# Performance work log

Measured on AMD Instinct MI355X. Metric: run time of the kernel, lower is better.

## Reference

```python
import jax, jax.numpy as jnp
import numpy as np

EPS = 1e-5

def hardsigmoid(x):
    # torch F.hardsigmoid: clip(x/6 + 0.5, 0, 1)
    return jnp.clip(x / 6.0 + 0.5, 0.0, 1.0)

def setup_inputs() -> dict:
    T, B, D = 2048, 8, 1024
    key = jax.random.key(0)
    k1, k2 = jax.random.split(key)
    x = jax.random.normal(k1, (T, B, D), dtype=jnp.float32)
    c = jnp.zeros((B, D), dtype=jnp.float32)
    # params
    w_ufr = jax.random.normal(k2, (3 * D, D), dtype=jnp.float32) * (1.0 / np.sqrt(D))
    gamma = jnp.ones((D,), dtype=jnp.float32)
    beta = jnp.zeros((D,), dtype=jnp.float32)
    return {"x": x, "c": c, "w_ufr": w_ufr, "gamma": gamma, "beta": beta}

def reference(x, c, w_ufr, gamma, beta):
    residual = x
    # LayerNorm over last dim
    mu = jnp.mean(x, axis=-1, keepdims=True)
    var = jnp.mean(jnp.square(x - mu), axis=-1, keepdims=True)
    x_norm = (x - mu) * jax.lax.rsqrt(var + EPS) * gamma + beta
    # fused projection to u, f, r: (T,B,D) @ (D,3D)
    ufr = jnp.einsum('tbd,ed->tbe', x_norm, w_ufr)
    u, f, r = jnp.split(ufr, 3, axis=-1)
    f_gate = hardsigmoid(f)
    r_gate = hardsigmoid(r)
    # diagonal linear recurrence: c_t = f_t * c_{t-1} + (1 - f_t) * u_t
    def step(c_prev, inputs):
        ft, ut = inputs
        c_curr = ft * c_prev + (1.0 - ft) * ut
        return c_curr, c_curr
    c_last, c_all = jax.lax.scan(step, c, (f_gate, u))
    tanh_approx = c_all / (1.0 + jnp.abs(c_all))  # softsign
    hs = r_gate * tanh_approx + (1.0 - r_gate) * x_norm
    return (residual + hs, c_last)
```

## Files before the change

### kernel.cpp

```cpp
#include <hip/hip_runtime.h>
#include <stdint.h>


#define T_SEQ 2048
#define BATCH 8
#define DIM 1024
#define M_SZ (T_SEQ * BATCH)
#define N_SZ (3 * DIM)
#define K_SZ DIM
#define NCHUNK 32
#define CLEN (T_SEQ / NCHUNK)

#define GBM 256
#define GBN 256
#define GBK 32
#define NKT (K_SZ / GBK)
#define NBX (N_SZ / GBN)
#define NWG (NBX * (M_SZ / GBM))

typedef __attribute__((ext_vector_type(8))) __bf16 bf16x8;
typedef __attribute__((ext_vector_type(4))) float f32x4;

__device__ __forceinline__ unsigned short f2bf(float f) {
  unsigned int u = __float_as_uint(f);
  u += 0x7FFFu + ((u >> 16) & 1u);
  return (unsigned short)(u >> 16);
}
__device__ __forceinline__ float bf2f(unsigned short s) {
  return __uint_as_float(((unsigned int)s) << 16);
}
__device__ __forceinline__ void gload16(const void* g, void* l) {
  __builtin_amdgcn_global_load_lds(
      (__attribute__((address_space(1))) void*)const_cast<void*>(g),
      (__attribute__((address_space(3))) void*)l, 16, 0, 0);
}

__global__ __launch_bounds__(256) void cvt_kernel(const float* __restrict__ w,
                                                  unsigned short* __restrict__ wb) {
  const int i = blockIdx.x * 256 + threadIdx.x;
  const float4 v = reinterpret_cast<const float4*>(w)[i];
  ushort4 o;
  o.x = f2bf(v.x); o.y = f2bf(v.y); o.z = f2bf(v.z); o.w = f2bf(v.w);
  reinterpret_cast<ushort4*>(wb)[i] = o;
}

__global__ __launch_bounds__(256) void ln_kernel(const float* __restrict__ x,
                                                 const float* __restrict__ gamma,
                                                 const float* __restrict__ beta,
                                                 unsigned short* __restrict__ xn,
                                                 float* __restrict__ muO,
                                                 float* __restrict__ rsO) {
  const int row = blockIdx.x;
  const int tid = threadIdx.x;
  const float4 v = reinterpret_cast<const float4*>(x + (size_t)row * DIM)[tid];
  float s = v.x + v.y + v.z + v.w;
  float q = v.x * v.x + v.y * v.y + v.z * v.z + v.w * v.w;
#pragma unroll
  for (int off = 32; off > 0; off >>= 1) {
    s += __shfl_down(s, off);
    q += __shfl_down(q, off);
  }
  __shared__ float sbuf[8];
  const int wv = tid >> 6, ln = tid & 63;
  if (ln == 0) { sbuf[wv] = s; sbuf[4 + wv] = q; }
  __syncthreads();
  s = sbuf[0] + sbuf[1] + sbuf[2] + sbuf[3];
  q = sbuf[4] + sbuf[5] + sbuf[6] + sbuf[7];
  const float mu = s * (1.0f / DIM);
  const float rstd = rsqrtf(q * (1.0f / DIM) - mu * mu + 1e-5f);
  if (tid == 0) { muO[row] = mu; rsO[row] = rstd; }
  const float4 g = reinterpret_cast<const float4*>(gamma)[tid];
  const float4 b = reinterpret_cast<const float4*>(beta)[tid];
  ushort4 o;
  o.x = f2bf((v.x - mu) * rstd * g.x + b.x);
  o.y = f2bf((v.y - mu) * rstd * g.y + b.y);
  o.z = f2bf((v.z - mu) * rstd * g.z + b.z);
  o.w = f2bf((v.w - mu) * rstd * g.w + b.w);
  reinterpret_cast<ushort4*>(xn + (size_t)row * DIM)[tid] = o;
}

__global__ __launch_bounds__(512) void gemm_kernel(const unsigned short* __restrict__ A,
                                                   const unsigned short* __restrict__ W,
                                                   unsigned short* __restrict__ U,
                                                   unsigned char* __restrict__ Fq,
                                                   unsigned char* __restrict__ Rq) {
  __shared__ unsigned short smem[2 * 4 * GBM * GBK];
  const int tid = threadIdx.x;
  const int lane = tid & 63;
  const int wid = tid >> 6;
  const int wm = wid >> 2, wn = wid & 3;

  const int wg = (blockIdx.x & 7) * (NWG / 8) + (blockIdx.x >> 3);
  const int bn0 = (wg % NBX) * GBN;
  const int bm0 = (wg / NBX) * GBM;

  const int stgRow = wid * 32 + (lane >> 2);
  const int stgCol = ((lane & 3) ^ ((lane >> 3) & 3)) * 8;
  const unsigned short* gA = A + (size_t)(bm0 + stgRow) * K_SZ + stgCol;
  const unsigned short* gB = W + (size_t)(bn0 + stgRow) * K_SZ + stgCol;
  unsigned short* sAb = smem + wid * 32 * GBK;
  unsigned short* sBb = smem + 4 * GBM * GBK + wid * 32 * GBK;

#define STAGE(bufi, t) do {                                        \
    const size_t ko_ = (size_t)(t) * GBK;                          \
    unsigned short* sa_ = sAb + (bufi) * (GBM * GBK);              \
    unsigned short* sb_ = sBb + (bufi) * (GBM * GBK);              \
    gload16(gA + ko_, sa_);                                        \
    gload16(gA + ko_ + (size_t)16 * K_SZ, sa_ + 16 * GBK);         \
    gload16(gB + ko_, sb_);                                        \
    gload16(gB + ko_ + (size_t)16 * K_SZ, sb_ + 16 * GBK);         \
  } while (0)

  f32x4 acc[8][4] = {};
  const int fr = lane & 15;
  const int ko8 = ((lane >> 4) ^ ((fr >> 1) & 3)) * 8;

  STAGE(0, 0);
  STAGE(1, 1);
  STAGE(2, 2);
  asm volatile("s_waitcnt vmcnt(8)" ::: "memory");
  __builtin_amdgcn_s_barrier();
  asm volatile("" ::: "memory");

  for (int kt = 0; kt < NKT; ++kt) {
    const int cur = kt & 3;
    if (kt < NKT - 3) STAGE((kt + 3) & 3, kt + 3);

    const unsigned short* sa = smem + cur * (GBM * GBK);
    const unsigned short* sb = smem + 4 * GBM * GBK + cur * (GBM * GBK);
    bf16x8 af[8], bf[4];
#pragma unroll
    for (int i = 0; i < 8; i++)
      af[i] = *(const bf16x8*)&sa[(wm * 128 + i * 16 + fr) * GBK + ko8];
#pragma unroll
    for (int j = 0; j < 4; j++)
      bf[j] = *(const bf16x8*)&sb[(wn * 64 + j * 16 + fr) * GBK + ko8];

    __builtin_amdgcn_s_setprio(1);
#pragma unroll
    for (int i = 0; i < 8; i++)
#pragma unroll
      for (int j = 0; j < 4; j++)
        acc[i][j] = __builtin_amdgcn_mfma_f32_16x16x32_bf16(af[i], bf[j], acc[i][j], 0, 0, 0);
    __builtin_amdgcn_s_setprio(0);

    if (kt < NKT - 3)       asm volatile("s_waitcnt vmcnt(8)" ::: "memory");
    else if (kt == NKT - 3) asm volatile("s_waitcnt vmcnt(4)" ::: "memory");
    else if (kt == NKT - 2) asm volatile("s_waitcnt vmcnt(0)" ::: "memory");
    if (kt < NKT - 1) {
      __builtin_amdgcn_s_barrier();
      asm volatile("" ::: "memory");
    }
  }
#undef STAGE

  const int region = bn0 >> 10;
  const int cb0 = bn0 & 1023;
  const int fq = lane >> 4;
  unsigned char* G = (region == 1) ? Fq : Rq;
#pragma unroll
  for (int i = 0; i < 8; i++) {
#pragma unroll
    for (int j = 0; j < 4; j++) {
      const int coln = cb0 + wn * 64 + j * 16 + fr;
      size_t base = (size_t)(bm0 + wm * 128 + i * 16 + fq * 4) * DIM + coln;
      if (region == 0) {
#pragma unroll
        for (int r = 0; r < 4; r++)
          U[base + (size_t)r * DIM] = f2bf(acc[i][j][r]);
      } else {
#pragma unroll
        for (int r = 0; r < 4; r++) {
          float v = fminf(fmaxf(acc[i][j][r] * (1.0f / 6.0f) + 0.5f, 0.0f), 1.0f);
          G[base + (size_t)r * DIM] = (unsigned char)(v * 255.0f + 0.5f);
        }
      }
    }
  }
}

__global__ __launch_bounds__(256) void scan1_kernel(const unsigned short* __restrict__ U,
                                                    const unsigned char* __restrict__ Fq,
                                                    float* __restrict__ Ac,
                                                    float* __restrict__ Bc) {
  const int lin = blockIdx.x * 256 + threadIdx.x;
  const int d0 = (lin & 255) << 2;
  const int b = (lin >> 8) & (BATCH - 1);
  const int g = lin >> 11;
  size_t off = (size_t)(g * CLEN) * (BATCH * DIM) + (size_t)b * DIM + d0;
  float Aa0 = 1.0f, Aa1 = 1.0f, Aa2 = 1.0f, Aa3 = 1.0f;
  float Bb0 = 0.0f, Bb1 = 0.0f, Bb2 = 0.0f, Bb3 = 0.0f;
#pragma unroll 4
  for (int t = 0; t < CLEN; t++) {
    const ushort4 uu = *reinterpret_cast<const ushort4*>(&U[off]);
    const uchar4 ff = *reinterpret_cast<const uchar4*>(&Fq[off]);
    const float f0 = ff.x * (1.0f / 255.0f), f1 = ff.y * (1.0f / 255.0f);
    const float f2 = ff.z * (1.0f / 255.0f), f3 = ff.w * (1.0f / 255.0f);
    Aa0 *= f0; Aa1 *= f1; Aa2 *= f2; Aa3 *= f3;
    Bb0 = f0 * Bb0 + (1.0f - f0) * bf2f(uu.x);
    Bb1 = f1 * Bb1 + (1.0f - f1) * bf2f(uu.y);
    Bb2 = f2 * Bb2 + (1.0f - f2) * bf2f(uu.z);
    Bb3 = f3 * Bb3 + (1.0f - f3) * bf2f(uu.w);
    off += BATCH * DIM;
  }
  const int o = g * (BATCH * DIM) + b * DIM + d0;
  *reinterpret_cast<float4*>(&Ac[o]) = make_float4(Aa0, Aa1, Aa2, Aa3);
  *reinterpret_cast<float4*>(&Bc[o]) = make_float4(Bb0, Bb1, Bb2, Bb3);
}

__global__ __launch_bounds__(256) void scan2_kernel(const float* __restrict__ Ac,
                                                    const float* __restrict__ Bc,
                                                    const float* __restrict__ c0,
                                                    float* __restrict__ cstart,
                                                    float* __restrict__ clast) {
  const int lin = blockIdx.x * 256 + threadIdx.x;
  float c = c0[lin];
#pragma unroll
  for (int g = 0; g < NCHUNK; g++) {
    cstart[g * (BATCH * DIM) + lin] = c;
    c = Ac[g * (BATCH * DIM) + lin] * c + Bc[g * (BATCH * DIM) + lin];
  }
  clast[lin] = c;
}

__global__ __launch_bounds__(256) void scan3_kernel(const unsigned short* __restrict__ U,
                                                    const unsigned char* __restrict__ Fq,
                                                    const unsigned char* __restrict__ Rq,
                                                    const float* __restrict__ x,
                                                    const float* __restrict__ cstart,
                                                    const float* __restrict__ muA,
                                                    const float* __restrict__ rsA,
                                                    const float* __restrict__ gamma,
                                                    const float* __restrict__ beta,
                                                    float* __restrict__ out) {
  const int lin = blockIdx.x * 256 + threadIdx.x;
  const int d0 = (lin & 255) << 2;
  const int b = (lin >> 8) & (BATCH - 1);
  const int g = lin >> 11;
  const float4 cs = *reinterpret_cast<const float4*>(&cstart[g * (BATCH * DIM) + b * DIM + d0]);
  float c0 = cs.x, c1 = cs.y, c2 = cs.z, c3 = cs.w;
  const float4 gm = *reinterpret_cast<const float4*>(&gamma[d0]);
  const float4 bt = *reinterpret_cast<const float4*>(&beta[d0]);
  size_t xo = (size_t)(g * CLEN) * (BATCH * DIM) + (size_t)b * DIM + d0;
  int row = g * CLEN * BATCH + b;
#pragma unroll 2
  for (int t = 0; t < CLEN; t++) {
    const ushort4 uu = *reinterpret_cast<const ushort4*>(&U[xo]);
    const uchar4 ff = *reinterpret_cast<const uchar4*>(&Fq[xo]);
    const uchar4 rr = *reinterpret_cast<const uchar4*>(&Rq[xo]);
    const float4 xv = *reinterpret_cast<const float4*>(&x[xo]);
    const float mu = muA[row], rs = rsA[row];
    float o[4];
    {
      const float f = ff.x * (1.0f / 255.0f), r = rr.x * (1.0f / 255.0f);
      const float xnv = (xv.x - mu) * rs * gm.x + bt.x;
      c0 = f * c0 + (1.0f - f) * bf2f(uu.x);
      o[0] = xv.x + r * (c0 / (1.0f + fabsf(c0))) + (1.0f - r) * xnv;
    }
    {
      const float f = ff.y * (1.0f / 255.0f), r = rr.y * (1.0f / 255.0f);
      const float xnv = (xv.y - mu) * rs * gm.y + bt.y;
      c1 = f * c1 + (1.0f - f) * bf2f(uu.y);
      o[1] = xv.y + r * (c1 / (1.0f + fabsf(c1))) + (1.0f - r) * xnv;
    }
    {
      const float f = ff.z * (1.0f / 255.0f), r = rr.z * (1.0f / 255.0f);
      const float xnv = (xv.z - mu) * rs * gm.z + bt.z;
      c2 = f * c2 + (1.0f - f) * bf2f(uu.z);
      o[2] = xv.z + r * (c2 / (1.0f + fabsf(c2))) + (1.0f - r) * xnv;
    }
    {
      const float f = ff.w * (1.0f / 255.0f), r = rr.w * (1.0f / 255.0f);
      const float xnv = (xv.w - mu) * rs * gm.w + bt.w;
      c3 = f * c3 + (1.0f - f) * bf2f(uu.w);
      o[3] = xv.w + r * (c3 / (1.0f + fabsf(c3))) + (1.0f - r) * xnv;
    }
    *reinterpret_cast<float4*>(&out[xo]) = make_float4(o[0], o[1], o[2], o[3]);
    xo += BATCH * DIM;
    row += BATCH;
  }
}

extern "C" void kernel_launch(void* const* d_in, const int* in_sizes, int n_in,
                              void* d_out, int out_size, void* d_ws, size_t ws_size,
                              hipStream_t stream) {
  const float* x = (const float*)d_in[0];
  const float* c0 = (const float*)d_in[1];
  const float* w = (const float*)d_in[2];
  const float* gamma = (const float*)d_in[3];
  const float* beta = (const float*)d_in[4];
  float* out = (float*)d_out;
  float* clast = out + (size_t)M_SZ * DIM;

  char* ws = (char*)d_ws;
  unsigned short* xn = (unsigned short*)ws;
  unsigned short* U  = (unsigned short*)(ws + 33554432ull);
  unsigned char* Fq  = (unsigned char*)(ws + 67108864ull);
  unsigned char* Rq  = (unsigned char*)(ws + 83886080ull);
  float* Ac = (float*)(ws + 100663296ull);
  float* Bc = (float*)(ws + 101711872ull);
  float* cst = (float*)(ws + 102760448ull);
  unsigned short* wb = (unsigned short*)(ws + 103809024ull);
  float* muA = (float*)(ws + 110100480ull);
  float* rsA = (float*)(ws + 110166016ull);

  cvt_kernel<<<(N_SZ * K_SZ / 4) / 256, 256, 0, stream>>>(w, wb);
  ln_kernel<<<M_SZ, 256, 0, stream>>>(x, gamma, beta, xn, muA, rsA);
  gemm_kernel<<<NWG, 512, 0, stream>>>(xn, wb, U, Fq, Rq);
  scan1_kernel<<<(NCHUNK * BATCH * DIM / 4) / 256, 256, 0, stream>>>(U, Fq, Ac, Bc);
  scan2_kernel<<<(BATCH * DIM) / 256, 256, 0, stream>>>(Ac, Bc, c0, cst, clast);
  scan3_kernel<<<(NCHUNK * BATCH * DIM / 4) / 256, 256, 0, stream>>>(
      U, Fq, Rq, x, cst, muA, rsA, gamma, beta, out);
}
```

Baseline: 193.6 us.

## Fuse three-pass chunked scan into single-pass decoupled look-back kernel

Replaces the three scan kernels with one kernel in which each chunk block computes its local aggregate, publishes it with status flags, and looks back over predecessor chunks to get its starting state before producing outputs. The weight bf16 conversion and LayerNorm are also merged into one launch. This removes launch gaps and the intermediate cstart round trip, and it lets the U and F reads for the second pass hit cache. In exchange it relies on spin-waiting inter-block flags. The flags need all predecessor blocks to be resident or scheduled in order (256 blocks here), and there is an extra memset.

```diff
diff --git a/kernel.cpp b/kernel.cpp
--- a/kernel.cpp
+++ b/kernel.cpp
@@ -18,6 +18,8 @@
 #define NBX (N_SZ / GBN)
 #define NWG (NBX * (M_SZ / GBM))
 
+#define CVT_BLOCKS ((N_SZ * K_SZ / 4) / 256)
+
 typedef __attribute__((ext_vector_type(8))) __bf16 bf16x8;
 typedef __attribute__((ext_vector_type(4))) float f32x4;
 
@@ -35,23 +37,24 @@
       (__attribute__((address_space(3))) void*)l, 16, 0, 0);
 }
 
-__global__ __launch_bounds__(256) void cvt_kernel(const float* __restrict__ w,
-                                                  unsigned short* __restrict__ wb) {
-  const int i = blockIdx.x * 256 + threadIdx.x;
-  const float4 v = reinterpret_cast<const float4*>(w)[i];
-  ushort4 o;
-  o.x = f2bf(v.x); o.y = f2bf(v.y); o.z = f2bf(v.z); o.w = f2bf(v.w);
-  reinterpret_cast<ushort4*>(wb)[i] = o;
-}
-
-__global__ __launch_bounds__(256) void ln_kernel(const float* __restrict__ x,
-                                                 const float* __restrict__ gamma,
-                                                 const float* __restrict__ beta,
-                                                 unsigned short* __restrict__ xn,
-                                                 float* __restrict__ muO,
-                                                 float* __restrict__ rsO) {
-  const int row = blockIdx.x;
+__global__ __launch_bounds__(256) void prep_kernel(const float* __restrict__ w,
+                                                   unsigned short* __restrict__ wb,
+                                                   const float* __restrict__ x,
+                                                   const float* __restrict__ gamma,
+                                                   const float* __restrict__ beta,
+                                                   unsigned short* __restrict__ xn,
+                                                   float* __restrict__ muO,
+                                                   float* __restrict__ rsO) {
   const int tid = threadIdx.x;
+  if (blockIdx.x < CVT_BLOCKS) {
+    const int i = blockIdx.x * 256 + tid;
+    const float4 v = reinterpret_cast<const float4*>(w)[i];
+    ushort4 o;
+    o.x = f2bf(v.x); o.y = f2bf(v.y); o.z = f2bf(v.z); o.w = f2bf(v.w);
+    reinterpret_cast<ushort4*>(wb)[i] = o;
+    return;
+  }
+  const int row = blockIdx.x - CVT_BLOCKS;
   const float4 v = reinterpret_cast<const float4*>(x + (size_t)row * DIM)[tid];
   float s = v.x + v.y + v.z + v.w;
   float q = v.x * v.x + v.y * v.y + v.z * v.z + v.w * v.w;
@@ -179,70 +182,113 @@
   }
 }
 
-__global__ __launch_bounds__(256) void scan1_kernel(const unsigned short* __restrict__ U,
-                                                    const unsigned char* __restrict__ Fq,
-                                                    float* __restrict__ Ac,
-                                                    float* __restrict__ Bc) {
-  const int lin = blockIdx.x * 256 + threadIdx.x;
-  const int d0 = (lin & 255) << 2;
-  const int b = (lin >> 8) & (BATCH - 1);
-  const int g = lin >> 11;
-  size_t off = (size_t)(g * CLEN) * (BATCH * DIM) + (size_t)b * DIM + d0;
+__global__ __launch_bounds__(256) void scan_fused(const unsigned short* __restrict__ U,
+                                                  const unsigned char* __restrict__ Fq,
+                                                  const unsigned char* __restrict__ Rq,
+                                                  const float* __restrict__ x,
+                                                  const float* __restrict__ cinit,
+                                                  const float* __restrict__ muA,
+                                                  const float* __restrict__ rsA,
+                                                  const float* __restrict__ gamma,
+                                                  const float* __restrict__ beta,
+                                                  float* __restrict__ aggA,
+                                                  float* __restrict__ aggB,
+                                                  float* __restrict__ inc,
+                                                  int* __restrict__ status,
+                                                  float* __restrict__ out,
+                                                  float* __restrict__ clast) {
+  const int blk = blockIdx.x;
+  const int g = blk >> 3;
+  const int s = blk & 7;
+  const int tid = threadIdx.x;
+  const int d0 = tid * 4;
+  const int ch = s * DIM + d0;
+
+  const size_t base = (size_t)(g * CLEN) * (BATCH * DIM) + (size_t)s * DIM + d0;
   float Aa0 = 1.0f, Aa1 = 1.0f, Aa2 = 1.0f, Aa3 = 1.0f;
   float Bb0 = 0.0f, Bb1 = 0.0f, Bb2 = 0.0f, Bb3 = 0.0f;
+  {
+    size_t off = base;
 #pragma unroll 4
-  for (int t = 0; t < CLEN; t++) {
-    const ushort4 uu = *reinterpret_cast<const ushort4*>(&U[off]);
-    const uchar4 ff = *reinterpret_cast<const uchar4*>(&Fq[off]);
-    const float f0 = ff.x * (1.0f / 255.0f), f1 = ff.y * (1.0f / 255.0f);
-    const float f2 = ff.z * (1.0f / 255.0f), f3 = ff.w * (1.0f / 255.0f);
-    Aa0 *= f0; Aa1 *= f1; Aa2 *= f2; Aa3 *= f3;
-    Bb0 = f0 * Bb0 + (1.0f - f0) * bf2f(uu.x);
-    Bb1 = f1 * Bb1 + (1.0f - f1) * bf2f(uu.y);
-    Bb2 = f2 * Bb2 + (1.0f - f2) * bf2f(uu.z);
-    Bb3 = f3 * Bb3 + (1.0f - f3) * bf2f(uu.w);
-    off += BATCH * DIM;
-  }
-  const int o = g * (BATCH * DIM) + b * DIM + d0;
-  *reinterpret_cast<float4*>(&Ac[o]) = make_float4(Aa0, Aa1, Aa2, Aa3);
-  *reinterpret_cast<float4*>(&Bc[o]) = make_float4(Bb0, Bb1, Bb2, Bb3);
-}
-
-__global__ __launch_bounds__(256) void scan2_kernel(const float* __restrict__ Ac,
-                                                    const float* __restrict__ Bc,
-                                                    const float* __restrict__ c0,
-                                                    float* __restrict__ cstart,
-                                                    float* __restrict__ clast) {
-  const int lin = blockIdx.x * 256 + threadIdx.x;
-  float c = c0[lin];
-#pragma unroll
-  for (int g = 0; g < NCHUNK; g++) {
-    cstart[g * (BATCH * DIM) + lin] = c;
-    c = Ac[g * (BATCH * DIM) + lin] * c + Bc[g * (BATCH * DIM) + lin];
-  }
-  clast[lin] = c;
-}
-
-__global__ __launch_bounds__(256) void scan3_kernel(const unsigned short* __restrict__ U,
-                                                    const unsigned char* __restrict__ Fq,
-                                                    const unsigned char* __restrict__ Rq,
-                                                    const float* __restrict__ x,
-                                                    const float* __restrict__ cstart,
-                                                    const float* __restrict__ muA,
-                                                    const float* __restrict__ rsA,
-                                                    const float* __restrict__ gamma,
-                                                    const float* __restrict__ beta,
-                                                    float* __restrict__ out) {
-  const int lin = blockIdx.x * 256 + threadIdx.x;
-  const int d0 = (lin & 255) << 2;
-  const int b = (lin >> 8) & (BATCH - 1);
-  const int g = lin >> 11;
-  const float4 cs = *reinterpret_cast<const float4*>(&cstart[g * (BATCH * DIM) + b * DIM + d0]);
-  float c0 = cs.x, c1 = cs.y, c2 = cs.z, c3 = cs.w;
+    for (int t = 0; t < CLEN; t++) {
+      const ushort4 uu = *reinterpret_cast<const ushort4*>(&U[off]);
+      const uchar4 ff = *reinterpret_cast<const uchar4*>(&Fq[off]);
+      const float f0 = ff.x * (1.0f / 255.0f), f1 = ff.y * (1.0f / 255.0f);
+      const float f2 = ff.z * (1.0f / 255.0f), f3 = ff.w * (1.0f / 255.0f);
+      Aa0 *= f0; Aa1 *= f1; Aa2 *= f2; Aa3 *= f3;
+      Bb0 = f0 * Bb0 + (1.0f - f0) * bf2f(uu.x);
+      Bb1 = f1 * Bb1 + (1.0f - f1) * bf2f(uu.y);
+      Bb2 = f2 * Bb2 + (1.0f - f2) * bf2f(uu.z);
+      Bb3 = f3 * Bb3 + (1.0f - f3) * bf2f(uu.w);
+      off += BATCH * DIM;
+    }
+  }
+
+  __shared__ int sh_st;
+  float cs0, cs1, cs2, cs3;
+  if (g == 0) {
+    const float4 cv = *reinterpret_cast<const float4*>(&cinit[ch]);
+    cs0 = cv.x; cs1 = cv.y; cs2 = cv.z; cs3 = cv.w;
+  } else {
+    const int go = g * (BATCH * DIM) + ch;
+    *reinterpret_cast<float4*>(&aggA[go]) = make_float4(Aa0, Aa1, Aa2, Aa3);
+    *reinterpret_cast<float4*>(&aggB[go]) = make_float4(Bb0, Bb1, Bb2, Bb3);
+    __threadfence();
+    __syncthreads();
+    if (tid == 0)
+      __hip_atomic_store(&status[blk], 1, __ATOMIC_RELEASE, __HIP_MEMORY_SCOPE_AGENT);
+
+    float Ka0 = 1.0f, Ka1 = 1.0f, Ka2 = 1.0f, Ka3 = 1.0f;
+    float Kb0 = 0.0f, Kb1 = 0.0f, Kb2 = 0.0f, Kb3 = 0.0f;
+    int j = g - 1;
+    for (;;) {
+      if (tid == 0) {
+        int v;
+        do {
+          v = __hip_atomic_load(&status[j * 8 + s], __ATOMIC_ACQUIRE,
+                                __HIP_MEMORY_SCOPE_AGENT);
+          if (v == 0) __builtin_amdgcn_s_sleep(2);
+        } while (v == 0);
+        sh_st = v;
+      }
+      __syncthreads();
+      const int v = sh_st;
+      __syncthreads();
+      const int jo = j * (BATCH * DIM) + ch;
+      if (v == 2) {
+        const float4 iv = *reinterpret_cast<const float4*>(&inc[jo]);
+        cs0 = Ka0 * iv.x + Kb0; cs1 = Ka1 * iv.y + Kb1;
+        cs2 = Ka2 * iv.z + Kb2; cs3 = Ka3 * iv.w + Kb3;
+        break;
+      }
+      const float4 av = *reinterpret_cast<const float4*>(&aggA[jo]);
+      const float4 bv = *reinterpret_cast<const float4*>(&aggB[jo]);
+      Kb0 = Ka0 * bv.x + Kb0; Ka0 = Ka0 * av.x;
+      Kb1 = Ka1 * bv.y + Kb1; Ka1 = Ka1 * av.y;
+      Kb2 = Ka2 * bv.z + Kb2; Ka2 = Ka2 * av.z;
+      Kb3 = Ka3 * bv.w + Kb3; Ka3 = Ka3 * av.w;
+      --j;
+    }
+  }
+
+  const float i0 = Aa0 * cs0 + Bb0, i1 = Aa1 * cs1 + Bb1;
+  const float i2 = Aa2 * cs2 + Bb2, i3 = Aa3 * cs3 + Bb3;
+  if (g < NCHUNK - 1) {
+    const int go = g * (BATCH * DIM) + ch;
+    *reinterpret_cast<float4*>(&inc[go]) = make_float4(i0, i1, i2, i3);
+    __threadfence();
+    __syncthreads();
+    if (tid == 0)
+      __hip_atomic_store(&status[blk], 2, __ATOMIC_RELEASE, __HIP_MEMORY_SCOPE_AGENT);
+  } else {
+    *reinterpret_cast<float4*>(&clast[ch]) = make_float4(i0, i1, i2, i3);
+  }
+
+  float c0 = cs0, c1 = cs1, c2 = cs2, c3 = cs3;
   const float4 gm = *reinterpret_cast<const float4*>(&gamma[d0]);
   const float4 bt = *reinterpret_cast<const float4*>(&beta[d0]);
-  size_t xo = (size_t)(g * CLEN) * (BATCH * DIM) + (size_t)b * DIM + d0;
-  int row = g * CLEN * BATCH + b;
+  size_t xo = base;
+  int row = g * CLEN * BATCH + s;
 #pragma unroll 2
   for (int t = 0; t < CLEN; t++) {
     const ushort4 uu = *reinterpret_cast<const ushort4*>(&U[xo]);
@@ -297,18 +343,18 @@
   unsigned short* U  = (unsigned short*)(ws + 33554432ull);
   unsigned char* Fq  = (unsigned char*)(ws + 67108864ull);
   unsigned char* Rq  = (unsigned char*)(ws + 83886080ull);
-  float* Ac = (float*)(ws + 100663296ull);
-  float* Bc = (float*)(ws + 101711872ull);
-  float* cst = (float*)(ws + 102760448ull);
+  float* aggA = (float*)(ws + 100663296ull);
+  float* aggB = (float*)(ws + 101711872ull);
+  float* inc  = (float*)(ws + 102760448ull);
   unsigned short* wb = (unsigned short*)(ws + 103809024ull);
   float* muA = (float*)(ws + 110100480ull);
   float* rsA = (float*)(ws + 110166016ull);
-
-  cvt_kernel<<<(N_SZ * K_SZ / 4) / 256, 256, 0, stream>>>(w, wb);
-  ln_kernel<<<M_SZ, 256, 0, stream>>>(x, gamma, beta, xn, muA, rsA);
+  int* status = (int*)(ws + 110231552ull);
+
+  hipMemsetAsync(status, 0, NCHUNK * BATCH * sizeof(int), stream);
+  prep_kernel<<<CVT_BLOCKS + M_SZ, 256, 0, stream>>>(w, wb, x, gamma, beta, xn, muA, rsA);
   gemm_kernel<<<NWG, 512, 0, stream>>>(xn, wb, U, Fq, Rq);
-  scan1_kernel<<<(NCHUNK * BATCH * DIM / 4) / 256, 256, 0, stream>>>(U, Fq, Ac, Bc);
-  scan2_kernel<<<(BATCH * DIM) / 256, 256, 0, stream>>>(Ac, Bc, c0, cst, clast);
-  scan3_kernel<<<(NCHUNK * BATCH * DIM / 4) / 256, 256, 0, stream>>>(
-      U, Fq, Rq, x, cst, muA, rsA, gamma, beta, out);
-}
+  scan_fused<<<NCHUNK * BATCH, 256, 0, stream>>>(U, Fq, Rq, x, c0, muA, rsA,
+                                                 gamma, beta, aggA, aggB, inc,
+                                                 status, out, clast);
+}
```

Result: slower. 267.2 us (+38.0%).
